# Performance work log

Hardware: AMD Instinct MI355X
Metric: run time of the kernel (lower is better)

The kernel has to match this reference:

```python
import jax, jax.numpy as jnp
import numpy as np

B, S, E, H, D = 64, 512, 512, 8, 64  # batch, n_steps, embedding_size, head_count, QKV_dim

def setup_inputs() -> dict:
    key = jax.random.key(0)
    ks = jax.random.split(key, 7)
    x = jax.random.normal(ks[0], (B, S, E), dtype=jnp.float32)
    mask = jax.random.randint(ks[1], (B, S), 0, 2).astype(jnp.float32)  # 1 = masked out
    WQ = jax.random.normal(ks[2], (H, E, D), dtype=jnp.float32) * 0.1
    WK = jax.random.normal(ks[3], (H, E, D), dtype=jnp.float32) * 0.1
    WV = jax.random.normal(ks[4], (H, E, D), dtype=jnp.float32) * 0.1
    BE = jax.random.normal(ks[5], (S, E), dtype=jnp.float32) * 0.1
    WO = jax.random.normal(ks[6], (H * D, E), dtype=jnp.float32) * 0.1
    return {"x": x, "mask": mask, "WQ": WQ, "WK": WK, "WV": WV, "BE": BE, "WO": WO}

def reference(x, mask, WQ, WK, WV, BE, WO):
    # add learned positional bias
    h = x + BE  # [B,S,E]
    # per-head projections, vectorized over heads
    Q = jnp.einsum('bse,hed->bhsd', h, WQ)
    K = jnp.einsum('bse,hed->bhsd', h, WK)
    V = jnp.einsum('bse,hed->bhsd', h, WV)
    # NOTE: original scales by sqrt(embedding_size), not sqrt(QKV_dim)
    scores = jnp.einsum('bhsd,bhtd->bhst', Q, K) / np.sqrt(E).astype(np.float32)
    # additive mask trick: mask tiled over query dim, key positions masked where mask==1
    scores = scores - mask[:, None, None, :] * 1e10
    alpha = jax.nn.softmax(scores, axis=-1)  # [B,H,S,S]
    attn = jnp.einsum('bhst,bhtd->bhsd', alpha, V)  # [B,H,S,D]
    # concat heads along feature dim -> [B,S,H*D], then output projection
    attn = jnp.transpose(attn, (0, 2, 1, 3)).reshape(x.shape[0], x.shape[1], -1)
    return attn @ WO  # [B,S,E]
```

## Files before the change

kernel.cpp:

```cpp
#include <hip/hip_runtime.h>
#include <hip/hip_bf16.h>


#define Bn 64
#define Sn 512
#define En 512
#define Hn 8
#define Dn 64

typedef __attribute__((ext_vector_type(8))) short s8v;
typedef __attribute__((ext_vector_type(4))) float f4v;

__device__ __forceinline__ unsigned short f2bf(float f) {
    union { float f; unsigned int u; } v; v.f = f;
    unsigned int u = v.u;
    u += 0x7fffu + ((u >> 16) & 1u);
    return (unsigned short)(u >> 16);
}

__device__ __forceinline__ void async16(const unsigned short* g, unsigned short* l) {
    __builtin_amdgcn_global_load_lds((const __attribute__((address_space(1))) void*)g,
                                     (__attribute__((address_space(3))) void*)l, 16, 0, 0);
}
__device__ __forceinline__ void async4(const float* g, float* l) {
    __builtin_amdgcn_global_load_lds((const __attribute__((address_space(1))) void*)g,
                                     (__attribute__((address_space(3))) void*)l, 4, 0, 0);
}

__global__ __launch_bounds__(256) void prep_h(const float* __restrict__ x,
                                              const float* __restrict__ BE,
                                              unsigned short* __restrict__ hbf) {
    int i = (blockIdx.x * 256 + threadIdx.x) * 4;
    int se = i % (Sn * En);
    float4 a = *(const float4*)(x + i);
    float4 b = *(const float4*)(BE + se);
    ushort4 o;
    o.x = f2bf(a.x + b.x); o.y = f2bf(a.y + b.y);
    o.z = f2bf(a.z + b.z); o.w = f2bf(a.w + b.w);
    *(ushort4*)(hbf + i) = o;
}

__global__ __launch_bounds__(256) void prep_w(const float* __restrict__ WQ,
                                              const float* __restrict__ WK,
                                              const float* __restrict__ WV,
                                              const float* __restrict__ WO,
                                              unsigned short* __restrict__ Wqkvt,
                                              unsigned short* __restrict__ WOt) {
    int idx = blockIdx.x * 256 + threadIdx.x;
    const int NW = 3 * Hn * Dn * En;
    if (idx < NW) {
        int e = idx & 511;
        int d = (idx >> 9) & 63;
        int h = (idx >> 15) & 7;
        int m = idx >> 18;
        const float* W = (m == 0) ? WQ : (m == 1) ? WK : WV;
        Wqkvt[idx] = f2bf(W[(h * En + e) * Dn + d]);
    } else {
        int j = idx - NW;
        int n = j & 511;
        int e = j >> 9;
        WOt[j] = f2bf(WO[n * En + e]);
    }
}

__global__ __launch_bounds__(256) void qkv_gemm(const unsigned short* __restrict__ hbf,
                                                const unsigned short* __restrict__ Wqkvt,
                                                unsigned short* __restrict__ Qo,
                                                unsigned short* __restrict__ Ko,
                                                unsigned short* __restrict__ Vt) {
    int nb = blockIdx.x, mb = blockIdx.y;
    __shared__ __align__(16) unsigned short At[128 * 64];
    __shared__ __align__(16) unsigned short Bt[128 * 64];
    int tid = threadIdx.x;
    int w = tid >> 6, lane = tid & 63, quad = lane >> 4, l16 = lane & 15;
    int wr = w >> 1, wc = w & 1;
    int lrow = lane >> 3;
    int lseg = ((lane & 7) ^ lrow) * 8;

    f4v acc[4][4];
#pragma unroll
    for (int i = 0; i < 4; i++)
#pragma unroll
        for (int n = 0; n < 4; n++) acc[i][n] = (f4v){0.f, 0.f, 0.f, 0.f};

    const unsigned short* Ag = hbf + (size_t)mb * 128 * 512;
    const unsigned short* Bg = Wqkvt + (size_t)nb * 128 * 512;

    for (int kc = 0; kc < 8; kc++) {
        __syncthreads();
#pragma unroll
        for (int i = 0; i < 4; i++) {
            int r0 = w * 32 + i * 8;
            async16(Ag + (r0 + lrow) * 512 + kc * 64 + lseg, &At[r0 * 64]);
            async16(Bg + (r0 + lrow) * 512 + kc * 64 + lseg, &Bt[r0 * 64]);
        }
        __syncthreads();
#pragma unroll
        for (int ks = 0; ks < 2; ks++) {
            int sw = ((ks * 4 + quad) ^ (l16 & 7)) * 8;
            s8v a[4], b[4];
#pragma unroll
            for (int i = 0; i < 4; i++)
                a[i] = *(const s8v*)&At[(wr * 64 + i * 16 + l16) * 64 + sw];
#pragma unroll
            for (int n = 0; n < 4; n++)
                b[n] = *(const s8v*)&Bt[(wc * 64 + n * 16 + l16) * 64 + sw];
#pragma unroll
            for (int i = 0; i < 4; i++)
#pragma unroll
                for (int n = 0; n < 4; n++)
                    acc[i][n] = __builtin_amdgcn_mfma_f32_16x16x32_bf16(a[i], b[n], acc[i][n], 0, 0, 0);
        }
    }

    int mat = nb >> 2;
    int h = (nb & 3) * 2 + wc;
    int b = mb >> 2;
    int s0 = (mb & 3) * 128 + wr * 64;
    const float qscale = 0.06375873f;

    if (mat < 2) {
        unsigned short* op = (mat == 0) ? Qo : Ko;
        float sc = (mat == 0) ? qscale : 1.0f;
#pragma unroll
        for (int i = 0; i < 4; i++)
#pragma unroll
            for (int n = 0; n < 4; n++)
#pragma unroll
                for (int r = 0; r < 4; r++) {
                    int s = s0 + i * 16 + quad * 4 + r;
                    int d = n * 16 + l16;
                    op[(size_t)((b * Hn + h) * Sn + s) * Dn + d] = f2bf(acc[i][n][r] * sc);
                }
    } else {
#pragma unroll
        for (int i = 0; i < 4; i++)
#pragma unroll
            for (int n = 0; n < 4; n++) {
                int d = n * 16 + l16;
                int s = s0 + i * 16 + quad * 4;
                ushort4 pk;
                pk.x = f2bf(acc[i][n][0]); pk.y = f2bf(acc[i][n][1]);
                pk.z = f2bf(acc[i][n][2]); pk.w = f2bf(acc[i][n][3]);
                *(ushort4*)&Vt[(size_t)((b * Hn + h) * Dn + d) * Sn + s] = pk;
            }
    }
}

__global__ __launch_bounds__(256) void attn_kernel(const unsigned short* __restrict__ Q,
                                                   const unsigned short* __restrict__ K,
                                                   const unsigned short* __restrict__ Vt,
                                                   const float* __restrict__ mask,
                                                   unsigned short* __restrict__ attn) {
    int qhalf = blockIdx.x, bh = blockIdx.y;
    int h = bh & 7, b = bh >> 3;
    __shared__ __align__(16) unsigned short Kc[64 * 64];
    __shared__ __align__(16) unsigned short Vc[64 * 64];
    __shared__ __align__(16) unsigned short Ps[4][4 * 16 * 64];
    __shared__ float maskv[64];
    int tid = threadIdx.x;
    int w = tid >> 6, lane = tid & 63, quad = lane >> 4, l16 = lane & 15;
    int l7 = l16 & 7;

    const unsigned short* Qg = Q + (size_t)(bh * Sn + qhalf * 256) * Dn;
    const unsigned short* Kg = K + (size_t)(bh * Sn) * Dn;
    const unsigned short* Vg = Vt + (size_t)(bh * Dn) * Sn;

    s8v aq[4][2];
#pragma unroll
    for (int i = 0; i < 4; i++)
#pragma unroll
        for (int ks = 0; ks < 2; ks++)
            aq[i][ks] = *(const s8v*)&Qg[((w * 4 + i) * 16 + l16) * 64 + ks * 32 + quad * 8];

    f4v acc[4][4];
    float psum[4] = {0.f, 0.f, 0.f, 0.f};
#pragma unroll
    for (int i = 0; i < 4; i++)
#pragma unroll
        for (int n = 0; n < 4; n++) acc[i][n] = (f4v){0.f, 0.f, 0.f, 0.f};

    int srow0 = w * 16 + (lane >> 3);
    int srow1 = srow0 + 8;
    int gseg0 = ((lane & 7) ^ (srow0 & 7)) * 8;
    int gseg1 = ((lane & 7) ^ (srow1 & 7)) * 8;
    unsigned short* kdst0 = &Kc[(w * 16) * 64];
    unsigned short* kdst1 = &Kc[(w * 16 + 8) * 64];
    unsigned short* vdst0 = &Vc[(w * 16) * 64];
    unsigned short* vdst1 = &Vc[(w * 16 + 8) * 64];

    unsigned short* Pw = Ps[w];
    int wbase = l16 * 64 + (quad & 1) * 4;
    const float cM = -1.4426950409e10f;

    for (int kc = 0; kc < 8; kc++) {
        __syncthreads();
        async16(Kg + (kc * 64 + srow0) * 64 + gseg0, kdst0);
        async16(Kg + (kc * 64 + srow1) * 64 + gseg1, kdst1);
        async16(Vg + srow0 * 512 + kc * 64 + gseg0, vdst0);
        async16(Vg + srow1 * 512 + kc * 64 + gseg1, vdst1);
        if (w == 0) async4(mask + b * Sn + kc * 64 + lane, maskv);
        __syncthreads();

#pragma unroll
        for (int n = 0; n < 4; n++) {
            s8v bk0 = *(const s8v*)&Kc[(n * 16 + l16) * 64 + (quad ^ l7) * 8];
            s8v bk1 = *(const s8v*)&Kc[(n * 16 + l16) * 64 + ((4 + quad) ^ l7) * 8];
            float4 mv = *(const float4*)&maskv[n * 16 + quad * 4];
            float m0 = mv.x * cM, m1 = mv.y * cM, m2 = mv.z * cM, m3 = mv.w * cM;
            int wseg = ((n * 2 + (quad >> 1)) ^ l7) * 8;
            f4v sacc[4];
#pragma unroll
            for (int i = 0; i < 4; i++) {
                sacc[i] = __builtin_amdgcn_mfma_f32_16x16x32_bf16(
                              bk0, aq[i][0], (f4v){0.f, 0.f, 0.f, 0.f}, 0, 0, 0);
                sacc[i] = __builtin_amdgcn_mfma_f32_16x16x32_bf16(
                              bk1, aq[i][1], sacc[i], 0, 0, 0);
            }
#pragma unroll
            for (int i = 0; i < 4; i++) {
                unsigned int u0 = __float_as_uint(__builtin_amdgcn_exp2f(sacc[i][0] + m0));
                unsigned int u1 = __float_as_uint(__builtin_amdgcn_exp2f(sacc[i][1] + m1));
                unsigned int u2 = __float_as_uint(__builtin_amdgcn_exp2f(sacc[i][2] + m2));
                unsigned int u3 = __float_as_uint(__builtin_amdgcn_exp2f(sacc[i][3] + m3));
                psum[i] += __uint_as_float(u0 & 0xffff0000u) + __uint_as_float(u1 & 0xffff0000u)
                         + __uint_as_float(u2 & 0xffff0000u) + __uint_as_float(u3 & 0xffff0000u);
                uint2 pk;
                pk.x = (u0 >> 16) | (u1 & 0xffff0000u);
                pk.y = (u2 >> 16) | (u3 & 0xffff0000u);
                *(uint2*)&Pw[(i << 10) + wbase + wseg] = pk;
            }
        }

#pragma unroll
        for (int ks = 0; ks < 2; ks++) {
            int sw = ((ks * 4 + quad) ^ l7) * 8;
            s8v ap[4];
#pragma unroll
            for (int i = 0; i < 4; i++)
                ap[i] = *(const s8v*)&Pw[(i << 10) + l16 * 64 + sw];
#pragma unroll
            for (int n = 0; n < 4; n++) {
                s8v bv = *(const s8v*)&Vc[(n * 16 + l16) * 64 + sw];
#pragma unroll
                for (int i = 0; i < 4; i++)
                    acc[i][n] = __builtin_amdgcn_mfma_f32_16x16x32_bf16(ap[i], bv, acc[i][n], 0, 0, 0);
            }
        }
    }

#pragma unroll
    for (int i = 0; i < 4; i++) {
        float s = psum[i];
        s += __shfl_xor(s, 16, 64);
        s += __shfl_xor(s, 32, 64);
        float inv[4];
#pragma unroll
        for (int r = 0; r < 4; r++)
            inv[r] = 1.0f / __shfl(s, quad * 4 + r, 64);
#pragma unroll
        for (int n = 0; n < 4; n++)
#pragma unroll
            for (int r = 0; r < 4; r++) {
                int query = qhalf * 256 + (w * 4 + i) * 16 + quad * 4 + r;
                int col = h * 64 + n * 16 + l16;
                attn[(size_t)(b * Sn + query) * (Hn * Dn) + col] = f2bf(acc[i][n][r] * inv[r]);
            }
    }
}

__global__ __launch_bounds__(256) void outproj(const unsigned short* __restrict__ attn,
                                               const unsigned short* __restrict__ WOt,
                                               float* __restrict__ out) {
    int nb = blockIdx.x, mb = blockIdx.y;
    __shared__ __align__(16) unsigned short At[128 * 64];
    __shared__ __align__(16) unsigned short Bt[128 * 64];
    int tid = threadIdx.x;
    int w = tid >> 6, lane = tid & 63, quad = lane >> 4, l16 = lane & 15;
    int wr = w >> 1, wc = w & 1;
    int lrow = lane >> 3;
    int lseg = ((lane & 7) ^ lrow) * 8;

    f4v acc[4][4];
#pragma unroll
    for (int i = 0; i < 4; i++)
#pragma unroll
        for (int n = 0; n < 4; n++) acc[i][n] = (f4v){0.f, 0.f, 0.f, 0.f};

    const unsigned short* Ag = attn + (size_t)mb * 128 * 512;
    const unsigned short* Bg = WOt + (size_t)nb * 128 * 512;

    for (int kc = 0; kc < 8; kc++) {
        __syncthreads();
#pragma unroll
        for (int i = 0; i < 4; i++) {
            int r0 = w * 32 + i * 8;
            async16(Ag + (r0 + lrow) * 512 + kc * 64 + lseg, &At[r0 * 64]);
            async16(Bg + (r0 + lrow) * 512 + kc * 64 + lseg, &Bt[r0 * 64]);
        }
        __syncthreads();
#pragma unroll
        for (int ks = 0; ks < 2; ks++) {
            int sw = ((ks * 4 + quad) ^ (l16 & 7)) * 8;
            s8v a[4], b[4];
#pragma unroll
            for (int i = 0; i < 4; i++)
                a[i] = *(const s8v*)&At[(wr * 64 + i * 16 + l16) * 64 + sw];
#pragma unroll
            for (int n = 0; n < 4; n++)
                b[n] = *(const s8v*)&Bt[(wc * 64 + n * 16 + l16) * 64 + sw];
#pragma unroll
            for (int i = 0; i < 4; i++)
#pragma unroll
                for (int n = 0; n < 4; n++)
                    acc[i][n] = __builtin_amdgcn_mfma_f32_16x16x32_bf16(a[i], b[n], acc[i][n], 0, 0, 0);
        }
    }
#pragma unroll
    for (int i = 0; i < 4; i++)
#pragma unroll
        for (int n = 0; n < 4; n++)
#pragma unroll
            for (int r = 0; r < 4; r++) {
                int row = mb * 128 + wr * 64 + i * 16 + quad * 4 + r;
                int col = nb * 128 + wc * 64 + n * 16 + l16;
                out[(size_t)row * 512 + col] = acc[i][n][r];
            }
}

extern "C" void kernel_launch(void* const* d_in, const int* in_sizes, int n_in,
                              void* d_out, int out_size, void* d_ws, size_t ws_size,
                              hipStream_t stream) {
    const float* x    = (const float*)d_in[0];
    const float* mask = (const float*)d_in[1];
    const float* WQ   = (const float*)d_in[2];
    const float* WK   = (const float*)d_in[3];
    const float* WV   = (const float*)d_in[4];
    const float* BE   = (const float*)d_in[5];
    const float* WO   = (const float*)d_in[6];
    float* out = (float*)d_out;

    char* ws = (char*)d_ws;
    unsigned short* hbf   = (unsigned short*)(ws);
    unsigned short* Wqkvt = (unsigned short*)(ws + 33554432);
    unsigned short* WOt   = (unsigned short*)(ws + 35127296);
    unsigned short* Qp    = (unsigned short*)(ws + 35651584);
    unsigned short* Kp    = (unsigned short*)(ws + 69206016);
    unsigned short* Vtp   = (unsigned short*)(ws + 102760448);
    unsigned short* attnp = (unsigned short*)(ws + 136314880);

    prep_h<<<16384, 256, 0, stream>>>(x, BE, hbf);
    prep_w<<<4096, 256, 0, stream>>>(WQ, WK, WV, WO, Wqkvt, WOt);
    qkv_gemm<<<dim3(12, 256), 256, 0, stream>>>(hbf, Wqkvt, Qp, Kp, Vtp);
    attn_kernel<<<dim3(2, 512), 256, 0, stream>>>(Qp, Kp, Vtp, mask, attnp);
    outproj<<<dim3(4, 256), 256, 0, stream>>>(attnp, WOt, out);
}
```

Measured before the change: 296.2 us.

## Double-buffer LDS in projection GEMMs and vectorize stores via swapped MFMA operands

Both the QKV and output-projection GEMMs now use two LDS buffers. The next K-chunk's async global-to-LDS loads are issued before computing on the current chunk, which removes one barrier per iteration and overlaps load latency with MFMA work. The MFMA operands are swapped (for the Q/K tiles and for the output projection) so each lane holds four contiguous columns of a row, allowing ushort4 and float4 stores instead of scalar ones. The cost is double the LDS per block (64KB), which may lower occupancy.

```diff
diff --git a/kernel.cpp b/kernel.cpp
--- a/kernel.cpp
+++ b/kernel.cpp
@@ -69,13 +69,14 @@
                                                 unsigned short* __restrict__ Ko,
                                                 unsigned short* __restrict__ Vt) {
     int nb = blockIdx.x, mb = blockIdx.y;
-    __shared__ __align__(16) unsigned short At[128 * 64];
-    __shared__ __align__(16) unsigned short Bt[128 * 64];
+    __shared__ __align__(16) unsigned short At[2][128 * 64];
+    __shared__ __align__(16) unsigned short Bt[2][128 * 64];
     int tid = threadIdx.x;
     int w = tid >> 6, lane = tid & 63, quad = lane >> 4, l16 = lane & 15;
     int wr = w >> 1, wc = w & 1;
     int lrow = lane >> 3;
     int lseg = ((lane & 7) ^ lrow) * 8;
+    bool swapQK = (nb < 8);
 
     f4v acc[4][4];
 #pragma unroll
@@ -86,31 +87,51 @@
     const unsigned short* Ag = hbf + (size_t)mb * 128 * 512;
     const unsigned short* Bg = Wqkvt + (size_t)nb * 128 * 512;
 
+#pragma unroll
+    for (int i = 0; i < 4; i++) {
+        int r0 = w * 32 + i * 8;
+        async16(Ag + (r0 + lrow) * 512 + lseg, &At[0][r0 * 64]);
+        async16(Bg + (r0 + lrow) * 512 + lseg, &Bt[0][r0 * 64]);
+    }
+    __syncthreads();
+
+    int cur = 0;
     for (int kc = 0; kc < 8; kc++) {
-        __syncthreads();
-#pragma unroll
-        for (int i = 0; i < 4; i++) {
-            int r0 = w * 32 + i * 8;
-            async16(Ag + (r0 + lrow) * 512 + kc * 64 + lseg, &At[r0 * 64]);
-            async16(Bg + (r0 + lrow) * 512 + kc * 64 + lseg, &Bt[r0 * 64]);
-        }
-        __syncthreads();
+        if (kc < 7) {
+            int nxt = cur ^ 1;
+#pragma unroll
+            for (int i = 0; i < 4; i++) {
+                int r0 = w * 32 + i * 8;
+                async16(Ag + (r0 + lrow) * 512 + (kc + 1) * 64 + lseg, &At[nxt][r0 * 64]);
+                async16(Bg + (r0 + lrow) * 512 + (kc + 1) * 64 + lseg, &Bt[nxt][r0 * 64]);
+            }
+        }
 #pragma unroll
         for (int ks = 0; ks < 2; ks++) {
             int sw = ((ks * 4 + quad) ^ (l16 & 7)) * 8;
             s8v a[4], b[4];
 #pragma unroll
             for (int i = 0; i < 4; i++)
-                a[i] = *(const s8v*)&At[(wr * 64 + i * 16 + l16) * 64 + sw];
+                a[i] = *(const s8v*)&At[cur][(wr * 64 + i * 16 + l16) * 64 + sw];
 #pragma unroll
             for (int n = 0; n < 4; n++)
-                b[n] = *(const s8v*)&Bt[(wc * 64 + n * 16 + l16) * 64 + sw];
-#pragma unroll
-            for (int i = 0; i < 4; i++)
-#pragma unroll
-                for (int n = 0; n < 4; n++)
-                    acc[i][n] = __builtin_amdgcn_mfma_f32_16x16x32_bf16(a[i], b[n], acc[i][n], 0, 0, 0);
-        }
+                b[n] = *(const s8v*)&Bt[cur][(wc * 64 + n * 16 + l16) * 64 + sw];
+            if (swapQK) {
+#pragma unroll
+                for (int i = 0; i < 4; i++)
+#pragma unroll
+                    for (int n = 0; n < 4; n++)
+                        acc[i][n] = __builtin_amdgcn_mfma_f32_16x16x32_bf16(b[n], a[i], acc[i][n], 0, 0, 0);
+            } else {
+#pragma unroll
+                for (int i = 0; i < 4; i++)
+#pragma unroll
+                    for (int n = 0; n < 4; n++)
+                        acc[i][n] = __builtin_amdgcn_mfma_f32_16x16x32_bf16(a[i], b[n], acc[i][n], 0, 0, 0);
+            }
+        }
+        if (kc < 7) __syncthreads();
+        cur ^= 1;
     }
 
     int mat = nb >> 2;
@@ -125,13 +146,16 @@
 #pragma unroll
         for (int i = 0; i < 4; i++)
 #pragma unroll
-            for (int n = 0; n < 4; n++)
-#pragma unroll
-                for (int r = 0; r < 4; r++) {
-                    int s = s0 + i * 16 + quad * 4 + r;
-                    int d = n * 16 + l16;
-                    op[(size_t)((b * Hn + h) * Sn + s) * Dn + d] = f2bf(acc[i][n][r] * sc);
-                }
+            for (int n = 0; n < 4; n++) {
+                int s = s0 + i * 16 + l16;
+                int d0 = n * 16 + quad * 4;
+                ushort4 pk;
+                pk.x = f2bf(acc[i][n][0] * sc);
+                pk.y = f2bf(acc[i][n][1] * sc);
+                pk.z = f2bf(acc[i][n][2] * sc);
+                pk.w = f2bf(acc[i][n][3] * sc);
+                *(ushort4*)&op[(size_t)((b * Hn + h) * Sn + s) * Dn + d0] = pk;
+            }
     } else {
 #pragma unroll
         for (int i = 0; i < 4; i++)
@@ -273,8 +297,8 @@
                                                const unsigned short* __restrict__ WOt,
                                                float* __restrict__ out) {
     int nb = blockIdx.x, mb = blockIdx.y;
-    __shared__ __align__(16) unsigned short At[128 * 64];
-    __shared__ __align__(16) unsigned short Bt[128 * 64];
+    __shared__ __align__(16) unsigned short At[2][128 * 64];
+    __shared__ __align__(16) unsigned short Bt[2][128 * 64];
     int tid = threadIdx.x;
     int w = tid >> 6, lane = tid & 63, quad = lane >> 4, l16 = lane & 15;
     int wr = w >> 1, wc = w & 1;
@@ -290,42 +314,55 @@
     const unsigned short* Ag = attn + (size_t)mb * 128 * 512;
     const unsigned short* Bg = WOt + (size_t)nb * 128 * 512;
 
+#pragma unroll
+    for (int i = 0; i < 4; i++) {
+        int r0 = w * 32 + i * 8;
+        async16(Ag + (r0 + lrow) * 512 + lseg, &At[0][r0 * 64]);
+        async16(Bg + (r0 + lrow) * 512 + lseg, &Bt[0][r0 * 64]);
+    }
+    __syncthreads();
+
+    int cur = 0;
     for (int kc = 0; kc < 8; kc++) {
-        __syncthreads();
-#pragma unroll
-        for (int i = 0; i < 4; i++) {
-            int r0 = w * 32 + i * 8;
-            async16(Ag + (r0 + lrow) * 512 + kc * 64 + lseg, &At[r0 * 64]);
-            async16(Bg + (r0 + lrow) * 512 + kc * 64 + lseg, &Bt[r0 * 64]);
-        }
-        __syncthreads();
+        if (kc < 7) {
+            int nxt = cur ^ 1;
+#pragma unroll
+            for (int i = 0; i < 4; i++) {
+                int r0 = w * 32 + i * 8;
+                async16(Ag + (r0 + lrow) * 512 + (kc + 1) * 64 + lseg, &At[nxt][r0 * 64]);
+                async16(Bg + (r0 + lrow) * 512 + (kc + 1) * 64 + lseg, &Bt[nxt][r0 * 64]);
+            }
+        }
 #pragma unroll
         for (int ks = 0; ks < 2; ks++) {
             int sw = ((ks * 4 + quad) ^ (l16 & 7)) * 8;
             s8v a[4], b[4];
 #pragma unroll
             for (int i = 0; i < 4; i++)
-                a[i] = *(const s8v*)&At[(wr * 64 + i * 16 + l16) * 64 + sw];
+                a[i] = *(const s8v*)&At[cur][(wr * 64 + i * 16 + l16) * 64 + sw];
 #pragma unroll
             for (int n = 0; n < 4; n++)
-                b[n] = *(const s8v*)&Bt[(wc * 64 + n * 16 + l16) * 64 + sw];
+                b[n] = *(const s8v*)&Bt[cur][(wc * 64 + n * 16 + l16) * 64 + sw];
 #pragma unroll
             for (int i = 0; i < 4; i++)
 #pragma unroll
                 for (int n = 0; n < 4; n++)
-                    acc[i][n] = __builtin_amdgcn_mfma_f32_16x16x32_bf16(a[i], b[n], acc[i][n], 0, 0, 0);
-        }
-    }
-#pragma unroll
-    for (int i = 0; i < 4; i++)
-#pragma unroll
-        for (int n = 0; n < 4; n++)
-#pragma unroll
-            for (int r = 0; r < 4; r++) {
-                int row = mb * 128 + wr * 64 + i * 16 + quad * 4 + r;
-                int col = nb * 128 + wc * 64 + n * 16 + l16;
-                out[(size_t)row * 512 + col] = acc[i][n][r];
-            }
+                    acc[i][n] = __builtin_amdgcn_mfma_f32_16x16x32_bf16(b[n], a[i], acc[i][n], 0, 0, 0);
+        }
+        if (kc < 7) __syncthreads();
+        cur ^= 1;
+    }
+#pragma unroll
+    for (int i = 0; i < 4; i++)
+#pragma unroll
+        for (int n = 0; n < 4; n++) {
+            int row = mb * 128 + wr * 64 + i * 16 + l16;
+            int col = nb * 128 + wc * 64 + n * 16 + quad * 4;
+            float4 o;
+            o.x = acc[i][n][0]; o.y = acc[i][n][1];
+            o.z = acc[i][n][2]; o.w = acc[i][n][3];
+            *(float4*)&out[(size_t)row * 512 + col] = o;
+        }
 }
 
 extern "C" void kernel_launch(void* const* d_in, const int* in_sizes, int n_in,
```

Result: slower. 307.8 us (+3.9%).
